# Kernel optimization log

Hardware: AMD Instinct MI355X
Metric: run time of the kernel (lower is better)

Reference implementation:

```python
import jax, jax.numpy as jnp
import numpy as np

B, S, D, H = 4, 1024, 1024, 16
DH = D // H
RD = float(np.sqrt(D))


def linear_vdp(mu_a, var_a, mu_b, var_b):
    # Product of two independent random matrices: E[AB], Var[AB] (elementwise)
    mean = mu_a @ mu_b
    var = var_a @ var_b + var_a @ (mu_b ** 2) + (mu_a ** 2) @ var_b
    return mean, var


def softmax_vdp(a, var_a):
    # p = softmax(a); variance via squared Jacobian J_ij = p_i(delta_ij - p_j):
    # var_out_i = p_i^2 * (sum_j p_j^2 var_j + var_i * (1 - 2 p_i))
    p = jax.nn.softmax(a, axis=-1)
    s = jnp.sum(p * p * var_a, axis=-1, keepdims=True)
    var_out = p * p * (s + var_a * (1.0 - 2.0 * p))
    return p, var_out


def setup_inputs() -> dict:
    key = jax.random.key(0)
    ks = jax.random.split(key, 8)
    x = jax.random.normal(ks[0], (B, S, D), dtype=jnp.float32)
    var_x = jax.random.uniform(ks[1], (B, S, D), dtype=jnp.float32) * 0.1
    k = jax.random.normal(ks[2], (B, H, S, DH), dtype=jnp.float32)
    var_k = jax.random.uniform(ks[3], (B, H, S, DH), dtype=jnp.float32) * 0.1
    v = jax.random.normal(ks[4], (B, H, S, DH), dtype=jnp.float32)
    var_v = jax.random.uniform(ks[5], (B, H, S, DH), dtype=jnp.float32) * 0.1
    # LinearVDP(d, d, bias=False): weight mean + (positive) weight variance
    Wq_mu = jax.random.normal(ks[6], (D, D), dtype=jnp.float32) / np.sqrt(D)
    Wq_var = jax.random.uniform(ks[7], (D, D), dtype=jnp.float32) * (0.1 / D)
    return {"x": x, "var_x": var_x, "k": k, "var_k": var_k, "v": v,
            "var_v": var_v, "Wq_mu": Wq_mu, "Wq_var": Wq_var}


def reference(x, var_x, k, var_k, v, var_v, Wq_mu, Wq_var):
    # LinearVDP projection (y = x W^T with random weight)
    q = x @ Wq_mu.T
    var_q = var_x @ Wq_var.T + var_x @ (Wq_mu ** 2).T + (x ** 2) @ Wq_var.T
    # split heads: [B,S,D] -> [B,H,S,DH]
    q = q.reshape(B, S, H, DH).transpose(0, 2, 1, 3)
    var_q = var_q.reshape(B, S, H, DH).transpose(0, 2, 1, 3)
    # scores with variance propagation
    a, var_a = linear_vdp(q, var_q, jnp.swapaxes(k, 2, 3), jnp.swapaxes(var_k, 2, 3))
    a = a / RD
    var_a = var_a / (RD ** 2)
    # causal mask (-inf above diagonal) on the mean path only
    causal = jnp.triu(jnp.ones((S, S), dtype=bool), k=1)
    a = jnp.where(causal, -jnp.inf, a)
    a, var_a = softmax_vdp(a, var_a)
    # attention * values with variance propagation
    a, var_a = linear_vdp(a, var_a, v, var_v)
    # merge heads: [B,H,S,DH] -> [B,S,D]
    a = a.transpose(0, 2, 1, 3).reshape(B, S, D)
    var_a = var_a.transpose(0, 2, 1, 3).reshape(B, S, D)
    return x + a, var_a
```

## Files before the change

### kernel.cpp

```cpp
#include <hip/hip_runtime.h>
#include <hip/hip_bf16.h>
#include <math.h>

#define NB 4
#define NS 1024
#define ND 1024
#define NH 16
#define NDH 64
#define M4 4194304
#define M1 1048576

typedef float f16v __attribute__((ext_vector_type(16)));
typedef short bf8 __attribute__((ext_vector_type(8)));
typedef unsigned short ushort_t;

union U8 { bf8 v; unsigned u[4]; unsigned short s[8]; };

__device__ __forceinline__ unsigned pk(float lo, float hi) {
    __hip_bfloat162 h2 = __float22bfloat162_rn(make_float2(lo, hi));
    return *reinterpret_cast<unsigned*>(&h2);
}
__device__ __forceinline__ unsigned short f2b(float f) {
    unsigned u = __float_as_uint(f);
    unsigned r = (u + 0x7fffu + ((u >> 16) & 1u)) >> 16;
    return (unsigned short)r;
}
__device__ __forceinline__ float b2f(unsigned short h) {
    return __uint_as_float(((unsigned)h) << 16);
}
__device__ __forceinline__ f16v zero16() {
    f16v z;
    #pragma unroll
    for (int i = 0; i < 16; ++i) z[i] = 0.f;
    return z;
}
__device__ __forceinline__ void vscale(f16v& v, float s) {
    #pragma unroll
    for (int i = 0; i < 16; ++i) v[i] *= s;
}

__device__ __forceinline__ void gl_lds16(const ushort_t* g, ushort_t* l) {
    __builtin_amdgcn_global_load_lds(
        (const __attribute__((address_space(1))) unsigned int*)g,
        (__attribute__((address_space(3))) unsigned int*)l,
        16, 0, 0);
}

__device__ __forceinline__ bf8 mkB(unsigned p0, unsigned p1, unsigned p2, unsigned p3, int h) {
    unsigned own0 = h ? p2 : p0;
    unsigned own1 = h ? p3 : p1;
    unsigned ct0  = h ? p0 : p2;
    unsigned ct1  = h ? p1 : p3;
    unsigned x0 = (unsigned)__shfl_xor((int)ct0, 32);
    unsigned x1 = (unsigned)__shfl_xor((int)ct1, 32);
    U8 B;
    B.u[0] = h ? x0 : own0;
    B.u[1] = h ? x1 : own1;
    B.u[2] = h ? own0 : x0;
    B.u[3] = h ? own1 : x1;
    return B.v;
}


__global__ __launch_bounds__(256)
void prep_xw(const float* __restrict__ x, const float* __restrict__ vx,
             const float* __restrict__ Wm, const float* __restrict__ Wv,
             ushort_t* __restrict__ fx, ushort_t* __restrict__ fvx, ushort_t* __restrict__ fx2,
             ushort_t* __restrict__ fm, ushort_t* __restrict__ fw2, ushort_t* __restrict__ fv)
{
    const size_t g = (size_t)blockIdx.x * 256 + threadIdx.x;
    if (g < 524288) {
        const size_t g0 = g * 8;
        const int row = (int)(g0 >> 10), k0 = (int)(g0 & 1023);
        const size_t fo = ((size_t)(row >> 5) * 64 + (k0 >> 4)) * 512
                        + ((row & 31) + 32 * ((k0 >> 3) & 1)) * 8;
        float a[8], c[8];
        *(float4*)(a)   = *(const float4*)(x + g0);  *(float4*)(a+4) = *(const float4*)(x + g0 + 4);
        *(float4*)(c)   = *(const float4*)(vx + g0); *(float4*)(c+4) = *(const float4*)(vx + g0 + 4);
        *(uint4*)(fx  + fo) = make_uint4(pk(a[0],a[1]), pk(a[2],a[3]), pk(a[4],a[5]), pk(a[6],a[7]));
        *(uint4*)(fvx + fo) = make_uint4(pk(c[0],c[1]), pk(c[2],c[3]), pk(c[4],c[5]), pk(c[6],c[7]));
        *(uint4*)(fx2 + fo) = make_uint4(pk(a[0]*a[0],a[1]*a[1]), pk(a[2]*a[2],a[3]*a[3]),
                                         pk(a[4]*a[4],a[5]*a[5]), pk(a[6]*a[6],a[7]*a[7]));
    } else {
        const size_t g0 = (g - 524288) * 8;
        const int row = (int)(g0 >> 10), k0 = (int)(g0 & 1023);
        const size_t fo = ((size_t)(row >> 5) * 64 + (k0 >> 4)) * 512
                        + ((row & 31) + 32 * ((k0 >> 3) & 1)) * 8;
        float a[8], c[8];
        *(float4*)(a)   = *(const float4*)(Wm + g0); *(float4*)(a+4) = *(const float4*)(Wm + g0 + 4);
        *(float4*)(c)   = *(const float4*)(Wv + g0); *(float4*)(c+4) = *(const float4*)(Wv + g0 + 4);
        *(uint4*)(fm  + fo) = make_uint4(pk(a[0],a[1]), pk(a[2],a[3]), pk(a[4],a[5]), pk(a[6],a[7]));
        *(uint4*)(fv  + fo) = make_uint4(pk(c[0],c[1]), pk(c[2],c[3]), pk(c[4],c[5]), pk(c[6],c[7]));
        *(uint4*)(fw2 + fo) = make_uint4(pk(fmaf(a[0],a[0],c[0]), fmaf(a[1],a[1],c[1])),
                                         pk(fmaf(a[2],a[2],c[2]), fmaf(a[3],a[3],c[3])),
                                         pk(fmaf(a[4],a[4],c[4]), fmaf(a[5],a[5],c[5])),
                                         pk(fmaf(a[6],a[6],c[6]), fmaf(a[7],a[7],c[7])));
    }
}

__global__ __launch_bounds__(256)
void prep_kv(const float* __restrict__ K,  const float* __restrict__ VK,
             const float* __restrict__ Vv, const float* __restrict__ VV,
             ushort_t* __restrict__ kmF, ushort_t* __restrict__ k2F, ushort_t* __restrict__ kvF,
             ushort_t* __restrict__ vmF, ushort_t* __restrict__ wF,  ushort_t* __restrict__ vvF)
{
    __shared__ ushort_t Lm[2048], Lw[2048], Lv[2048];
    const int tid = threadIdx.x;
    const int bh = blockIdx.x, s = blockIdx.y;
    const int jp  = tid >> 3;
    const int dh0 = (tid & 7) * 8;
    const size_t gin = ((size_t)bh * NS + s * 32 + jp) * NDH + dh0;
    const size_t sbase = ((size_t)bh * 32 + s) * 2048;

    float kk[8], uu[8], vm[8], vv[8];
    *(float4*)(kk)   = *(const float4*)(K  + gin); *(float4*)(kk+4) = *(const float4*)(K  + gin + 4);
    *(float4*)(uu)   = *(const float4*)(VK + gin); *(float4*)(uu+4) = *(const float4*)(VK + gin + 4);
    *(float4*)(vm)   = *(const float4*)(Vv + gin); *(float4*)(vm+4) = *(const float4*)(Vv + gin + 4);
    *(float4*)(vv)   = *(const float4*)(VV + gin); *(float4*)(vv+4) = *(const float4*)(VV + gin + 4);

    const size_t kout = sbase + (size_t)((tid & 7) >> 1) * 512
                      + (jp + 32 * ((tid & 7) & 1)) * 8;
    unsigned o0[4], o1[4], o2[4];
    #pragma unroll
    for (int t = 0; t < 4; ++t) {
        o0[t] = pk(kk[2*t], kk[2*t+1]);
        o1[t] = pk(fmaf(kk[2*t],kk[2*t],uu[2*t]), fmaf(kk[2*t+1],kk[2*t+1],uu[2*t+1]));
        o2[t] = pk(uu[2*t], uu[2*t+1]);
    }
    *(uint4*)(kmF + kout) = make_uint4(o0[0],o0[1],o0[2],o0[3]);
    *(uint4*)(k2F + kout) = make_uint4(o1[0],o1[1],o1[2],o1[3]);
    *(uint4*)(kvF + kout) = make_uint4(o2[0],o2[1],o2[2],o2[3]);

    #pragma unroll
    for (int e = 0; e < 8; ++e) {
        const int dh = dh0 + e;
        const int idx = ((dh >> 5) * 2 + (jp >> 4)) * 512
                      + ((dh & 31) + 32 * ((jp >> 3) & 1)) * 8 + (jp & 7);
        Lm[idx] = f2b(vm[e]);
        Lw[idx] = f2b(fmaf(vm[e], vm[e], vv[e]));
        Lv[idx] = f2b(vv[e]);
    }
    __syncthreads();
    const size_t vout = sbase + (size_t)tid * 8;
    *(uint4*)(vmF + vout) = *(const uint4*)(Lm + tid * 8);
    *(uint4*)(wF  + vout) = *(const uint4*)(Lw + tid * 8);
    *(uint4*)(vvF + vout) = *(const uint4*)(Lv + tid * 8);
}

__global__ __launch_bounds__(256, 2)
void qproj_b(const ushort_t* __restrict__ xplanes,
             const ushort_t* __restrict__ wplanes,
             ushort_t* __restrict__ qmF, ushort_t* __restrict__ vqF)
{
    __shared__ ushort_t wstg[2][12 * 512];

    const int tid  = threadIdx.x;
    const int w    = tid >> 6;
    const int lane = tid & 63;
    const int lh   = lane & 31;
    const int h    = lane >> 5;
    const int head = blockIdx.x;
    const int mb   = blockIdx.y;
    const int mt   = mb * 4 + w;
    const int nt   = head * 2 + (w & 1);

    f16v aQ0 = zero16(), aQ1 = zero16(), aV0 = zero16(), aV1 = zero16();

    const ushort_t* xb = xplanes + (size_t)mt * 64 * 512 + lane * 8;
    const ushort_t* wsrc = wplanes + ((size_t)nt * 64 + (w >> 1)) * 512 + lane * 8;

    #pragma unroll
    for (int q = 0; q < 3; ++q)
        gl_lds16(wsrc + (size_t)q * M1, &wstg[0][(3 * w + q) * 512 + lane * 8]);
    __syncthreads();

    for (int t = 0; t < 32; ++t) {
        const int cur = t & 1;
        if (t + 1 < 32) {
            #pragma unroll
            for (int q = 0; q < 3; ++q)
                gl_lds16(wsrc + (size_t)q * M1 + (size_t)(2 * (t + 1)) * 512,
                         &wstg[cur ^ 1][(3 * w + q) * 512 + lane * 8]);
        }
        const ushort_t* sc = wstg[cur];
        #pragma unroll
        for (int kcL = 0; kcL < 2; ++kcL) {
            const int off = (2 * t + kcL) * 512;
            bf8 bx  = *(const bf8*)(xb + 0 * (size_t)M4 + off);
            bf8 bvx = *(const bf8*)(xb + 1 * (size_t)M4 + off);
            bf8 bx2 = *(const bf8*)(xb + 2 * (size_t)M4 + off);
            bf8 A0m = *(const bf8*)(sc + (3 * (2 * kcL + 0) + 0) * 512 + lane * 8);
            bf8 A0w = *(const bf8*)(sc + (3 * (2 * kcL + 0) + 1) * 512 + lane * 8);
            bf8 A0v = *(const bf8*)(sc + (3 * (2 * kcL + 0) + 2) * 512 + lane * 8);
            bf8 A1m = *(const bf8*)(sc + (3 * (2 * kcL + 1) + 0) * 512 + lane * 8);
            bf8 A1w = *(const bf8*)(sc + (3 * (2 * kcL + 1) + 1) * 512 + lane * 8);
            bf8 A1v = *(const bf8*)(sc + (3 * (2 * kcL + 1) + 2) * 512 + lane * 8);
            aQ0 = __builtin_amdgcn_mfma_f32_32x32x16_bf16(A0m, bx,  aQ0, 0, 0, 0);
            aV0 = __builtin_amdgcn_mfma_f32_32x32x16_bf16(A0w, bvx, aV0, 0, 0, 0);
            aV0 = __builtin_amdgcn_mfma_f32_32x32x16_bf16(A0v, bx2, aV0, 0, 0, 0);
            aQ1 = __builtin_amdgcn_mfma_f32_32x32x16_bf16(A1m, bx,  aQ1, 0, 0, 0);
            aV1 = __builtin_amdgcn_mfma_f32_32x32x16_bf16(A1w, bvx, aV1, 0, 0, 0);
            aV1 = __builtin_amdgcn_mfma_f32_32x32x16_bf16(A1v, bx2, aV1, 0, 0, 0);
        }
        __syncthreads();
    }

    const int mrow = mt * 32 + lh;
    const int b = mrow >> 10;
    const int rt = mt & 31;
    const size_t bh_base = ((size_t)(b * NH + head)) * 65536 + (size_t)rt * 2048;
    const float S1 = 0.03125f, S2 = 0.0009765625f;
    #pragma unroll
    for (int i = 0; i < 16; i += 2) {
        const int dh0 = (i & 3) + 8 * (i >> 2) + 4 * h;
        const size_t o = bh_base + (size_t)(dh0 >> 4) * 512
                       + (lh + 32 * ((dh0 >> 3) & 1)) * 8 + (dh0 & 7);
        *(unsigned*)(qmF + o)         = pk(aQ0[i]*S1, aQ0[i+1]*S1);
        *(unsigned*)(qmF + o + 1024)  = pk(aQ1[i]*S1, aQ1[i+1]*S1);
        *(unsigned*)(vqF + o)         = pk(aV0[i]*S2, aV0[i+1]*S2);
        *(unsigned*)(vqF + o + 1024)  = pk(aV1[i]*S2, aV1[i+1]*S2);
    }
}

__global__ __launch_bounds__(256, 2)
void attn_b(const ushort_t* __restrict__ qmF, const ushort_t* __restrict__ vqF,
            const ushort_t* __restrict__ planes,
            const float* __restrict__ x,
            float* __restrict__ out0, float* __restrict__ out1)
{
    __shared__ union {
        ushort_t stg[2][6 * 2048];
        float ep[128][66];
    } sm;

    const int tid  = threadIdx.x;
    const int w    = tid >> 6;
    const int lane = tid & 63;
    const int lh   = lane & 31;
    const int h    = lane >> 5;
    const int blk  = blockIdx.x;
    const int lb   = (blk & 7) * 64 + (blk >> 3);
    const int rb   = 7 - (lb & 7);
    const int bh   = lb >> 3;
    const int rt   = rb * 4 + w;
    const size_t base = (size_t)bh * 65536;

    bf8 fqm[4], fvq[4], fq2[4];
    {
        const ushort_t* qp = qmF + base + (size_t)rt * 2048 + lane * 8;
        const ushort_t* vp = vqF + base + (size_t)rt * 2048 + lane * 8;
        #pragma unroll
        for (int c = 0; c < 4; ++c) {
            fqm[c] = *(const bf8*)(qp + c * 512);
            fvq[c] = *(const bf8*)(vp + c * 512);
            U8 t; t.v = fqm[c];
            U8 r;
            #pragma unroll
            for (int k = 0; k < 4; ++k) {
                float q0 = b2f(t.s[2*k]), q1 = b2f(t.s[2*k+1]);
                r.u[k] = pk(q0*q0, q1*q1);
            }
            fq2[c] = r.v;
        }
    }

    f16v aN1[2], aN2w[2], aM2[2], aN3[2];
    #pragma unroll
    for (int dt = 0; dt < 2; ++dt) { aN1[dt]=zero16(); aN2w[dt]=zero16(); aM2[dt]=zero16(); aN3[dt]=zero16(); }
    float mrun = -INFINITY, Zrun = 0.f, S2run = 0.f;

    const int nstage = 4 * rb + 4;
    #pragma unroll
    for (int p = 0; p < 6; ++p)
        gl_lds16(planes + (size_t)p * M4 + base + w * 512 + lane * 8,
                 &sm.stg[0][p * 2048 + w * 512 + lane * 8]);
    __syncthreads();

    for (int st = 0; st < nstage; ++st) {
        const int cur = st & 1;
        if (st + 1 < nstage) {
            #pragma unroll
            for (int p = 0; p < 6; ++p)
                gl_lds16(planes + (size_t)p * M4 + base + (size_t)(st + 1) * 2048 + w * 512 + lane * 8,
                         &sm.stg[cur ^ 1][p * 2048 + w * 512 + lane * 8]);
        }
        if (st <= rt) {
            const ushort_t* sb = sm.stg[cur];
            f16v accA = zero16(), accU = zero16();
            #pragma unroll
            for (int c = 0; c < 4; ++c) {
                bf8 A0 = *(const bf8*)(sb + 0 * 2048 + c * 512 + lane * 8);
                bf8 A1 = *(const bf8*)(sb + 1 * 2048 + c * 512 + lane * 8);
                bf8 A2 = *(const bf8*)(sb + 2 * 2048 + c * 512 + lane * 8);
                accA = __builtin_amdgcn_mfma_f32_32x32x16_bf16(A0, fqm[c], accA, 0, 0, 0);
                accU = __builtin_amdgcn_mfma_f32_32x32x16_bf16(A1, fvq[c], accU, 0, 0, 0);
                accU = __builtin_amdgcn_mfma_f32_32x32x16_bf16(A2, fq2[c], accU, 0, 0, 0);
            }
            if (st == rt) {
                #pragma unroll
                for (int i = 0; i < 16; ++i) {
                    const int jl = (i & 3) + 8 * (i >> 2) + 4 * h;
                    if (jl > lh) accA[i] = -INFINITY;
                }
            }
            float mx = accA[0];
            #pragma unroll
            for (int i = 1; i < 16; ++i) mx = fmaxf(mx, accA[i]);
            mx = fmaxf(mx, __shfl_xor(mx, 32));
            if (!__all(mx <= mrun + 8.f)) {
                const float mnew = fmaxf(mrun, mx);
                const float s1 = __expf(mrun - mnew);
                const float s2 = s1 * s1, s3 = s2 * s1;
                Zrun *= s1; S2run *= s2;
                #pragma unroll
                for (int dt = 0; dt < 2; ++dt) { vscale(aN1[dt],s1); vscale(aN2w[dt],s2); vscale(aM2[dt],s2); vscale(aN3[dt],s3); }
                mrun = mnew;
            }
            float Zt = 0.f, St = 0.f;
            #pragma unroll
            for (int i = 0; i < 16; ++i) {
                const float e = __expf(accA[i] - mrun);
                accA[i] = e;
                Zt += e; St = fmaf(e * e, accU[i], St);
            }
            Zt += __shfl_xor(Zt, 32); St += __shfl_xor(St, 32);
            Zrun += Zt; S2run += St;

            #pragma unroll
            for (int c2 = 0; c2 < 2; ++c2) {
                unsigned pE[4], pE2[4], pEU[4], pE3[4];
                #pragma unroll
                for (int k = 0; k < 4; ++k) {
                    const int i0 = 8*c2 + 2*k;
                    const float e0 = accA[i0], e1 = accA[i0+1];
                    const float q0 = e0*e0, q1 = e1*e1;
                    const float t0 = q0*accU[i0], t1 = q1*accU[i0+1];
                    pE [k] = pk(e0, e1);
                    pE2[k] = pk(q0, q1);
                    pEU[k] = pk(t0, t1);
                    pE3[k] = pk(t0*e0, t1*e1);
                }
                bf8 BE  = mkB(pE [0], pE [1], pE [2], pE [3], h);
                bf8 BE2 = mkB(pE2[0], pE2[1], pE2[2], pE2[3], h);
                bf8 BEU = mkB(pEU[0], pEU[1], pEU[2], pEU[3], h);
                bf8 BE3 = mkB(pE3[0], pE3[1], pE3[2], pE3[3], h);
                #pragma unroll
                for (int dt = 0; dt < 2; ++dt) {
                    const int vo = (3 + (dt * 2 + c2) / 4 * 0) * 0;
                    (void)vo;
                    const ushort_t* vp = sb + 3 * 2048 + (dt * 2 + c2) * 512 + lane * 8;
                    bf8 Am = *(const bf8*)(vp + 0 * 2048);
                    bf8 Aw = *(const bf8*)(vp + 1 * 2048);
                    bf8 Av = *(const bf8*)(vp + 2 * 2048);
                    aN1[dt]  = __builtin_amdgcn_mfma_f32_32x32x16_bf16(Am, BE,  aN1[dt],  0, 0, 0);
                    aN2w[dt] = __builtin_amdgcn_mfma_f32_32x32x16_bf16(Aw, BE2, aN2w[dt], 0, 0, 0);
                    aM2[dt]  = __builtin_amdgcn_mfma_f32_32x32x16_bf16(Aw, BEU, aM2[dt],  0, 0, 0);
                    aM2[dt]  = __builtin_amdgcn_mfma_f32_32x32x16_bf16(Av, BE2, aM2[dt],  0, 0, 0);
                    aN3[dt]  = __builtin_amdgcn_mfma_f32_32x32x16_bf16(Aw, BE3, aN3[dt],  0, 0, 0);
                }
            }
        }
        __syncthreads();
    }

    const float rZ  = 1.f / Zrun;
    const float rZ2 = rZ * rZ;
    const float sS  = S2run * rZ2;
    const int b = bh >> 4, head = bh & 15;

    #pragma unroll
    for (int dt = 0; dt < 2; ++dt)
        #pragma unroll
        for (int i = 0; i < 16; ++i) {
            const int col = 32*dt + (i & 3) + 8*(i >> 2) + 4*h;
            sm.ep[w*32 + lh][col] = aN1[dt][i] * rZ;
        }
    __syncthreads();
    {
        const int row = tid >> 1, half = (tid & 1) * 32;
        const size_t o = ((size_t)b * NS + rb*128 + row) * ND + head * NDH + half;
        #pragma unroll
        for (int q4 = 0; q4 < 32; q4 += 4) {
            float4 t = make_float4(sm.ep[row][half+q4], sm.ep[row][half+q4+1],
                                   sm.ep[row][half+q4+2], sm.ep[row][half+q4+3]);
            float4 xi = *(const float4*)(x + o + q4);
            *(float4*)(out0 + o + q4) = make_float4(t.x+xi.x, t.y+xi.y, t.z+xi.z, t.w+xi.w);
        }
    }
    __syncthreads();
    #pragma unroll
    for (int dt = 0; dt < 2; ++dt)
        #pragma unroll
        for (int i = 0; i < 16; ++i) {
            const int col = 32*dt + (i & 3) + 8*(i >> 2) + 4*h;
            sm.ep[w*32 + lh][col] = rZ2 * fmaf(sS, aN2w[dt][i], aM2[dt][i]) - 2.f*rZ2*rZ*aN3[dt][i];
        }
    __syncthreads();
    {
        const int row = tid >> 1, half = (tid & 1) * 32;
        const size_t o = ((size_t)b * NS + rb*128 + row) * ND + head * NDH + half;
        #pragma unroll
        for (int q4 = 0; q4 < 32; q4 += 4) {
            float4 t = make_float4(sm.ep[row][half+q4], sm.ep[row][half+q4+1],
                                   sm.ep[row][half+q4+2], sm.ep[row][half+q4+3]);
            *(float4*)(out1 + o + q4) = t;
        }
    }
}

extern "C" void kernel_launch(void* const* d_in, const int* in_sizes, int n_in,
                              void* d_out, int out_size, void* d_ws, size_t ws_size,
                              hipStream_t stream)
{
    (void)in_sizes; (void)n_in; (void)out_size; (void)ws_size;
    const float* x  = (const float*)d_in[0];
    const float* vx = (const float*)d_in[1];
    const float* K  = (const float*)d_in[2];
    const float* VK = (const float*)d_in[3];
    const float* Vv = (const float*)d_in[4];
    const float* VV = (const float*)d_in[5];
    const float* Wm = (const float*)d_in[6];
    const float* Wv = (const float*)d_in[7];

    float* out0 = (float*)d_out;
    float* out1 = out0 + (size_t)NB * NS * ND;

    ushort_t* qm  = (ushort_t*)d_ws;
    ushort_t* vq  = qm  + M4;
    ushort_t* kmF = vq  + M4;
    ushort_t* k2F = kmF + M4;
    ushort_t* kvF = k2F + M4;
    ushort_t* vmF = kvF + M4;
    ushort_t* wF  = vmF + M4;
    ushort_t* vvF = wF  + M4;
    ushort_t* fxF = vvF + M4;
    ushort_t* fvxF= fxF + M4;
    ushort_t* fx2F= fvxF+ M4;
    ushort_t* fmF = fx2F+ M4;
    ushort_t* fw2F= fmF + M1;
    ushort_t* fvF = fw2F+ M1;
    (void)k2F; (void)kvF; (void)vmF; (void)wF; (void)vvF; (void)fvxF; (void)fx2F; (void)fw2F; (void)fvF;

    prep_xw<<<2560, 256, 0, stream>>>(x, vx, Wm, Wv, fxF, fvxF, fx2F, fmF, fw2F, fvF);
    prep_kv<<<dim3(64, 32), 256, 0, stream>>>(K, VK, Vv, VV, kmF, k2F, kvF, vmF, wF, vvF);
    qproj_b<<<dim3(NH, 32), 256, 0, stream>>>(fxF, fmF, qm, vq);
    attn_b<<<512, 256, 0, stream>>>(qm, vq, kmF, x, out0, out1);
}
```

Before: 177.8 us.

## Triple-buffer LDS staging in qproj and attention, merge prep kernels

Both GEMM-style kernels (qproj_b, attn_b) go from double- to triple-buffered LDS staging, prefetching two stages ahead. The full __syncthreads is replaced by explicit vmcnt waits and raw s_barrier with sched_barrier fences, so global loads overlap more compute. The two prep kernels are also merged into one launch to save launch overhead and a tail. The cost is more shared memory per block, which may lower occupancy in attn_b (its stg buffer grows by half), plus reliance on hand-counted vmcnt values being correct.

```diff
diff --git a/kernel.cpp b/kernel.cpp
--- a/kernel.cpp
+++ b/kernel.cpp
@@ -63,88 +63,89 @@
 
 
 __global__ __launch_bounds__(256)
-void prep_xw(const float* __restrict__ x, const float* __restrict__ vx,
-             const float* __restrict__ Wm, const float* __restrict__ Wv,
-             ushort_t* __restrict__ fx, ushort_t* __restrict__ fvx, ushort_t* __restrict__ fx2,
-             ushort_t* __restrict__ fm, ushort_t* __restrict__ fw2, ushort_t* __restrict__ fv)
-{
-    const size_t g = (size_t)blockIdx.x * 256 + threadIdx.x;
-    if (g < 524288) {
-        const size_t g0 = g * 8;
-        const int row = (int)(g0 >> 10), k0 = (int)(g0 & 1023);
-        const size_t fo = ((size_t)(row >> 5) * 64 + (k0 >> 4)) * 512
-                        + ((row & 31) + 32 * ((k0 >> 3) & 1)) * 8;
-        float a[8], c[8];
-        *(float4*)(a)   = *(const float4*)(x + g0);  *(float4*)(a+4) = *(const float4*)(x + g0 + 4);
-        *(float4*)(c)   = *(const float4*)(vx + g0); *(float4*)(c+4) = *(const float4*)(vx + g0 + 4);
-        *(uint4*)(fx  + fo) = make_uint4(pk(a[0],a[1]), pk(a[2],a[3]), pk(a[4],a[5]), pk(a[6],a[7]));
-        *(uint4*)(fvx + fo) = make_uint4(pk(c[0],c[1]), pk(c[2],c[3]), pk(c[4],c[5]), pk(c[6],c[7]));
-        *(uint4*)(fx2 + fo) = make_uint4(pk(a[0]*a[0],a[1]*a[1]), pk(a[2]*a[2],a[3]*a[3]),
-                                         pk(a[4]*a[4],a[5]*a[5]), pk(a[6]*a[6],a[7]*a[7]));
-    } else {
-        const size_t g0 = (g - 524288) * 8;
-        const int row = (int)(g0 >> 10), k0 = (int)(g0 & 1023);
-        const size_t fo = ((size_t)(row >> 5) * 64 + (k0 >> 4)) * 512
-                        + ((row & 31) + 32 * ((k0 >> 3) & 1)) * 8;
-        float a[8], c[8];
-        *(float4*)(a)   = *(const float4*)(Wm + g0); *(float4*)(a+4) = *(const float4*)(Wm + g0 + 4);
-        *(float4*)(c)   = *(const float4*)(Wv + g0); *(float4*)(c+4) = *(const float4*)(Wv + g0 + 4);
-        *(uint4*)(fm  + fo) = make_uint4(pk(a[0],a[1]), pk(a[2],a[3]), pk(a[4],a[5]), pk(a[6],a[7]));
-        *(uint4*)(fv  + fo) = make_uint4(pk(c[0],c[1]), pk(c[2],c[3]), pk(c[4],c[5]), pk(c[6],c[7]));
-        *(uint4*)(fw2 + fo) = make_uint4(pk(fmaf(a[0],a[0],c[0]), fmaf(a[1],a[1],c[1])),
-                                         pk(fmaf(a[2],a[2],c[2]), fmaf(a[3],a[3],c[3])),
-                                         pk(fmaf(a[4],a[4],c[4]), fmaf(a[5],a[5],c[5])),
-                                         pk(fmaf(a[6],a[6],c[6]), fmaf(a[7],a[7],c[7])));
-    }
-}
-
-__global__ __launch_bounds__(256)
-void prep_kv(const float* __restrict__ K,  const float* __restrict__ VK,
-             const float* __restrict__ Vv, const float* __restrict__ VV,
-             ushort_t* __restrict__ kmF, ushort_t* __restrict__ k2F, ushort_t* __restrict__ kvF,
-             ushort_t* __restrict__ vmF, ushort_t* __restrict__ wF,  ushort_t* __restrict__ vvF)
+void prep_all(const float* __restrict__ x, const float* __restrict__ vx,
+              const float* __restrict__ K,  const float* __restrict__ VK,
+              const float* __restrict__ Vv, const float* __restrict__ VV,
+              const float* __restrict__ Wm, const float* __restrict__ Wv,
+              ushort_t* __restrict__ kmF, ushort_t* __restrict__ k2F, ushort_t* __restrict__ kvF,
+              ushort_t* __restrict__ vmF, ushort_t* __restrict__ wF,  ushort_t* __restrict__ vvF,
+              ushort_t* __restrict__ fx, ushort_t* __restrict__ fvx, ushort_t* __restrict__ fx2,
+              ushort_t* __restrict__ fm, ushort_t* __restrict__ fw2, ushort_t* __restrict__ fv)
 {
     __shared__ ushort_t Lm[2048], Lw[2048], Lv[2048];
     const int tid = threadIdx.x;
-    const int bh = blockIdx.x, s = blockIdx.y;
-    const int jp  = tid >> 3;
-    const int dh0 = (tid & 7) * 8;
-    const size_t gin = ((size_t)bh * NS + s * 32 + jp) * NDH + dh0;
-    const size_t sbase = ((size_t)bh * 32 + s) * 2048;
-
-    float kk[8], uu[8], vm[8], vv[8];
-    *(float4*)(kk)   = *(const float4*)(K  + gin); *(float4*)(kk+4) = *(const float4*)(K  + gin + 4);
-    *(float4*)(uu)   = *(const float4*)(VK + gin); *(float4*)(uu+4) = *(const float4*)(VK + gin + 4);
-    *(float4*)(vm)   = *(const float4*)(Vv + gin); *(float4*)(vm+4) = *(const float4*)(Vv + gin + 4);
-    *(float4*)(vv)   = *(const float4*)(VV + gin); *(float4*)(vv+4) = *(const float4*)(VV + gin + 4);
-
-    const size_t kout = sbase + (size_t)((tid & 7) >> 1) * 512
-                      + (jp + 32 * ((tid & 7) & 1)) * 8;
-    unsigned o0[4], o1[4], o2[4];
-    #pragma unroll
-    for (int t = 0; t < 4; ++t) {
-        o0[t] = pk(kk[2*t], kk[2*t+1]);
-        o1[t] = pk(fmaf(kk[2*t],kk[2*t],uu[2*t]), fmaf(kk[2*t+1],kk[2*t+1],uu[2*t+1]));
-        o2[t] = pk(uu[2*t], uu[2*t+1]);
-    }
-    *(uint4*)(kmF + kout) = make_uint4(o0[0],o0[1],o0[2],o0[3]);
-    *(uint4*)(k2F + kout) = make_uint4(o1[0],o1[1],o1[2],o1[3]);
-    *(uint4*)(kvF + kout) = make_uint4(o2[0],o2[1],o2[2],o2[3]);
-
-    #pragma unroll
-    for (int e = 0; e < 8; ++e) {
-        const int dh = dh0 + e;
-        const int idx = ((dh >> 5) * 2 + (jp >> 4)) * 512
-                      + ((dh & 31) + 32 * ((jp >> 3) & 1)) * 8 + (jp & 7);
-        Lm[idx] = f2b(vm[e]);
-        Lw[idx] = f2b(fmaf(vm[e], vm[e], vv[e]));
-        Lv[idx] = f2b(vv[e]);
-    }
-    __syncthreads();
-    const size_t vout = sbase + (size_t)tid * 8;
-    *(uint4*)(vmF + vout) = *(const uint4*)(Lm + tid * 8);
-    *(uint4*)(wF  + vout) = *(const uint4*)(Lw + tid * 8);
-    *(uint4*)(vvF + vout) = *(const uint4*)(Lv + tid * 8);
+    const int bid = blockIdx.x;
+
+    if (bid < 2048) {
+        const int bh = bid >> 5, s = bid & 31;
+        const int jp  = tid >> 3;
+        const int dh0 = (tid & 7) * 8;
+        const size_t gin = ((size_t)bh * NS + s * 32 + jp) * NDH + dh0;
+        const size_t sbase = ((size_t)bh * 32 + s) * 2048;
+
+        float kk[8], uu[8], vm[8], vv[8];
+        *(float4*)(kk)   = *(const float4*)(K  + gin); *(float4*)(kk+4) = *(const float4*)(K  + gin + 4);
+        *(float4*)(uu)   = *(const float4*)(VK + gin); *(float4*)(uu+4) = *(const float4*)(VK + gin + 4);
+        *(float4*)(vm)   = *(const float4*)(Vv + gin); *(float4*)(vm+4) = *(const float4*)(Vv + gin + 4);
+        *(float4*)(vv)   = *(const float4*)(VV + gin); *(float4*)(vv+4) = *(const float4*)(VV + gin + 4);
+
+        const size_t kout = sbase + (size_t)((tid & 7) >> 1) * 512
+                          + (jp + 32 * ((tid & 7) & 1)) * 8;
+        unsigned o0[4], o1[4], o2[4];
+        #pragma unroll
+        for (int t = 0; t < 4; ++t) {
+            o0[t] = pk(kk[2*t], kk[2*t+1]);
+            o1[t] = pk(fmaf(kk[2*t],kk[2*t],uu[2*t]), fmaf(kk[2*t+1],kk[2*t+1],uu[2*t+1]));
+            o2[t] = pk(uu[2*t], uu[2*t+1]);
+        }
+        *(uint4*)(kmF + kout) = make_uint4(o0[0],o0[1],o0[2],o0[3]);
+        *(uint4*)(k2F + kout) = make_uint4(o1[0],o1[1],o1[2],o1[3]);
+        *(uint4*)(kvF + kout) = make_uint4(o2[0],o2[1],o2[2],o2[3]);
+
+        #pragma unroll
+        for (int e = 0; e < 8; ++e) {
+            const int dh = dh0 + e;
+            const int idx = ((dh >> 5) * 2 + (jp >> 4)) * 512
+                          + ((dh & 31) + 32 * ((jp >> 3) & 1)) * 8 + (jp & 7);
+            Lm[idx] = f2b(vm[e]);
+            Lw[idx] = f2b(fmaf(vm[e], vm[e], vv[e]));
+            Lv[idx] = f2b(vv[e]);
+        }
+        __syncthreads();
+        const size_t vout = sbase + (size_t)tid * 8;
+        *(uint4*)(vmF + vout) = *(const uint4*)(Lm + tid * 8);
+        *(uint4*)(wF  + vout) = *(const uint4*)(Lw + tid * 8);
+        *(uint4*)(vvF + vout) = *(const uint4*)(Lv + tid * 8);
+    } else {
+        const size_t g = (size_t)(bid - 2048) * 256 + tid;
+        if (g < 524288) {
+            const size_t g0 = g * 8;
+            const int row = (int)(g0 >> 10), k0 = (int)(g0 & 1023);
+            const size_t fo = ((size_t)(row >> 5) * 64 + (k0 >> 4)) * 512
+                            + ((row & 31) + 32 * ((k0 >> 3) & 1)) * 8;
+            float a[8], c[8];
+            *(float4*)(a)   = *(const float4*)(x + g0);  *(float4*)(a+4) = *(const float4*)(x + g0 + 4);
+            *(float4*)(c)   = *(const float4*)(vx + g0); *(float4*)(c+4) = *(const float4*)(vx + g0 + 4);
+            *(uint4*)(fx  + fo) = make_uint4(pk(a[0],a[1]), pk(a[2],a[3]), pk(a[4],a[5]), pk(a[6],a[7]));
+            *(uint4*)(fvx + fo) = make_uint4(pk(c[0],c[1]), pk(c[2],c[3]), pk(c[4],c[5]), pk(c[6],c[7]));
+            *(uint4*)(fx2 + fo) = make_uint4(pk(a[0]*a[0],a[1]*a[1]), pk(a[2]*a[2],a[3]*a[3]),
+                                             pk(a[4]*a[4],a[5]*a[5]), pk(a[6]*a[6],a[7]*a[7]));
+        } else {
+            const size_t g0 = (g - 524288) * 8;
+            const int row = (int)(g0 >> 10), k0 = (int)(g0 & 1023);
+            const size_t fo = ((size_t)(row >> 5) * 64 + (k0 >> 4)) * 512
+                            + ((row & 31) + 32 * ((k0 >> 3) & 1)) * 8;
+            float a[8], c[8];
+            *(float4*)(a)   = *(const float4*)(Wm + g0); *(float4*)(a+4) = *(const float4*)(Wm + g0 + 4);
+            *(float4*)(c)   = *(const float4*)(Wv + g0); *(float4*)(c+4) = *(const float4*)(Wv + g0 + 4);
+            *(uint4*)(fm  + fo) = make_uint4(pk(a[0],a[1]), pk(a[2],a[3]), pk(a[4],a[5]), pk(a[6],a[7]));
+            *(uint4*)(fv  + fo) = make_uint4(pk(c[0],c[1]), pk(c[2],c[3]), pk(c[4],c[5]), pk(c[6],c[7]));
+            *(uint4*)(fw2 + fo) = make_uint4(pk(fmaf(a[0],a[0],c[0]), fmaf(a[1],a[1],c[1])),
+                                             pk(fmaf(a[2],a[2],c[2]), fmaf(a[3],a[3],c[3])),
+                                             pk(fmaf(a[4],a[4],c[4]), fmaf(a[5],a[5],c[5])),
+                                             pk(fmaf(a[6],a[6],c[6]), fmaf(a[7],a[7],c[7])));
+        }
+    }
 }
 
 __global__ __launch_bounds__(256, 2)
@@ -152,7 +153,7 @@
              const ushort_t* __restrict__ wplanes,
              ushort_t* __restrict__ qmF, ushort_t* __restrict__ vqF)
 {
-    __shared__ ushort_t wstg[2][12 * 512];
+    __shared__ ushort_t wstg[3][12 * 512];
 
     const int tid  = threadIdx.x;
     const int w    = tid >> 6;
@@ -172,16 +173,27 @@
     #pragma unroll
     for (int q = 0; q < 3; ++q)
         gl_lds16(wsrc + (size_t)q * M1, &wstg[0][(3 * w + q) * 512 + lane * 8]);
-    __syncthreads();
+    #pragma unroll
+    for (int q = 0; q < 3; ++q)
+        gl_lds16(wsrc + (size_t)q * M1 + 2 * 512, &wstg[1][(3 * w + q) * 512 + lane * 8]);
 
     for (int t = 0; t < 32; ++t) {
-        const int cur = t & 1;
-        if (t + 1 < 32) {
+        const int cur = t % 3;
+        if (t + 2 < 32) {
+            const int nxt = (t + 2) % 3;
             #pragma unroll
             for (int q = 0; q < 3; ++q)
-                gl_lds16(wsrc + (size_t)q * M1 + (size_t)(2 * (t + 1)) * 512,
-                         &wstg[cur ^ 1][(3 * w + q) * 512 + lane * 8]);
-        }
+                gl_lds16(wsrc + (size_t)q * M1 + (size_t)(2 * (t + 2)) * 512,
+                         &wstg[nxt][(3 * w + q) * 512 + lane * 8]);
+            asm volatile("s_waitcnt vmcnt(6)" ::: "memory");
+        } else if (t + 1 < 32) {
+            asm volatile("s_waitcnt vmcnt(3)" ::: "memory");
+        } else {
+            asm volatile("s_waitcnt vmcnt(0)" ::: "memory");
+        }
+        __builtin_amdgcn_s_barrier();
+        __builtin_amdgcn_sched_barrier(0);
+
         const ushort_t* sc = wstg[cur];
         #pragma unroll
         for (int kcL = 0; kcL < 2; ++kcL) {
@@ -202,7 +214,8 @@
             aV1 = __builtin_amdgcn_mfma_f32_32x32x16_bf16(A1w, bvx, aV1, 0, 0, 0);
             aV1 = __builtin_amdgcn_mfma_f32_32x32x16_bf16(A1v, bx2, aV1, 0, 0, 0);
         }
-        __syncthreads();
+        __builtin_amdgcn_sched_barrier(0);
+        __builtin_amdgcn_s_barrier();
     }
 
     const int mrow = mt * 32 + lh;
@@ -229,7 +242,7 @@
             float* __restrict__ out0, float* __restrict__ out1)
 {
     __shared__ union {
-        ushort_t stg[2][6 * 2048];
+        ushort_t stg[3][6 * 2048];
         float ep[128][66];
     } sm;
 
@@ -274,16 +287,28 @@
     for (int p = 0; p < 6; ++p)
         gl_lds16(planes + (size_t)p * M4 + base + w * 512 + lane * 8,
                  &sm.stg[0][p * 2048 + w * 512 + lane * 8]);
-    __syncthreads();
+    #pragma unroll
+    for (int p = 0; p < 6; ++p)
+        gl_lds16(planes + (size_t)p * M4 + base + 2048 + w * 512 + lane * 8,
+                 &sm.stg[1][p * 2048 + w * 512 + lane * 8]);
 
     for (int st = 0; st < nstage; ++st) {
-        const int cur = st & 1;
-        if (st + 1 < nstage) {
+        const int cur = st % 3;
+        if (st + 2 < nstage) {
+            const int nxt = (st + 2) % 3;
             #pragma unroll
             for (int p = 0; p < 6; ++p)
-                gl_lds16(planes + (size_t)p * M4 + base + (size_t)(st + 1) * 2048 + w * 512 + lane * 8,
-                         &sm.stg[cur ^ 1][p * 2048 + w * 512 + lane * 8]);
-        }
+                gl_lds16(planes + (size_t)p * M4 + base + (size_t)(st + 2) * 2048 + w * 512 + lane * 8,
+                         &sm.stg[nxt][p * 2048 + w * 512 + lane * 8]);
+            asm volatile("s_waitcnt vmcnt(12)" ::: "memory");
+        } else if (st + 1 < nstage) {
+            asm volatile("s_waitcnt vmcnt(6)" ::: "memory");
+        } else {
+            asm volatile("s_waitcnt vmcnt(0)" ::: "memory");
+        }
+        __builtin_amdgcn_s_barrier();
+        __builtin_amdgcn_sched_barrier(0);
+
         if (st <= rt) {
             const ushort_t* sb = sm.stg[cur];
             f16v accA = zero16(), accU = zero16();
@@ -346,8 +371,6 @@
                 bf8 BE3 = mkB(pE3[0], pE3[1], pE3[2], pE3[3], h);
                 #pragma unroll
                 for (int dt = 0; dt < 2; ++dt) {
-                    const int vo = (3 + (dt * 2 + c2) / 4 * 0) * 0;
-                    (void)vo;
                     const ushort_t* vp = sb + 3 * 2048 + (dt * 2 + c2) * 512 + lane * 8;
                     bf8 Am = *(const bf8*)(vp + 0 * 2048);
                     bf8 Aw = *(const bf8*)(vp + 1 * 2048);
@@ -360,7 +383,8 @@
                 }
             }
         }
-        __syncthreads();
+        __builtin_amdgcn_sched_barrier(0);
+        __builtin_amdgcn_s_barrier();
     }
 
     const float rZ  = 1.f / Zrun;
@@ -439,10 +463,10 @@
     ushort_t* fmF = fx2F+ M4;
     ushort_t* fw2F= fmF + M1;
     ushort_t* fvF = fw2F+ M1;
-    (void)k2F; (void)kvF; (void)vmF; (void)wF; (void)vvF; (void)fvxF; (void)fx2F; (void)fw2F; (void)fvF;
-
-    prep_xw<<<2560, 256, 0, stream>>>(x, vx, Wm, Wv, fxF, fvxF, fx2F, fmF, fw2F, fvF);
-    prep_kv<<<dim3(64, 32), 256, 0, stream>>>(K, VK, Vv, VV, kmF, k2F, kvF, vmF, wF, vvF);
+
+    prep_all<<<4608, 256, 0, stream>>>(x, vx, K, VK, Vv, VV, Wm, Wv,
+                                       kmF, k2F, kvF, vmF, wF, vvF,
+                                       fxF, fvxF, fx2F, fmF, fw2F, fvF);
     qproj_b<<<dim3(NH, 32), 256, 0, stream>>>(fxF, fmF, qm, vq);
     attn_b<<<512, 256, 0, stream>>>(qm, vq, kmF, x, out0, out1);
 }
```

New measurement: 168.4 us. 5.2% less time.
